# Optimization experiments

Hardware: AMD Instinct MI355X
Metric: run time of the kernel (lower is better)

Reference implementation:

```python
import jax, jax.numpy as jnp
import numpy as np
import math

B, S, DIM = 2, 2048, 2048
NH = 16
HD = DIM // NH  # 128
RANK = 32


def setup_inputs() -> dict:
    key = jax.random.key(0)
    ks = jax.random.split(key, 10)
    x = jax.random.normal(ks[0], (B, S, DIM), dtype=jnp.float32)
    # causal additive mask (use -1e9 instead of -inf for grad-safety)
    mask = jnp.where(jnp.tril(jnp.ones((S, S), dtype=bool)), 0.0, -1e9).astype(jnp.float32)[None, None]
    # rotary frequencies, as in llama: theta = 10000^{-2i/d}
    inv_freq = 1.0 / (10000.0 ** (jnp.arange(0, HD, 2, dtype=jnp.float32) / HD))  # [HD/2]
    t = jnp.arange(S, dtype=jnp.float32)
    freqs = jnp.outer(t, inv_freq)  # [S, HD/2]
    freqs_cos = jnp.cos(freqs)
    freqs_sin = jnp.sin(freqs)
    scale = 0.02
    wq = jax.random.normal(ks[1], (DIM, DIM), dtype=jnp.float32) * scale
    wk = jax.random.normal(ks[2], (DIM, DIM), dtype=jnp.float32) * scale
    wv = jax.random.normal(ks[3], (DIM, DIM), dtype=jnp.float32) * scale
    wo = jax.random.normal(ks[4], (DIM, DIM), dtype=jnp.float32) * scale
    wa_q = jax.random.normal(ks[5], (RANK, DIM), dtype=jnp.float32) * 0.02
    wa_k = jax.random.normal(ks[6], (RANK, DIM), dtype=jnp.float32) * 0.02
    return {"x": x, "mask": mask, "freqs_cos": freqs_cos, "freqs_sin": freqs_sin,
            "wq": wq, "wk": wk, "wv": wv, "wo": wo, "wa_q": wa_q, "wa_k": wa_k}


def _apply_rope(t, cos, sin):
    # t: [B, S, H, HD]; cos/sin: [S, HD/2]
    tr = t.reshape(*t.shape[:-1], HD // 2, 2)
    tre, tim = tr[..., 0], tr[..., 1]
    c = cos[None, :, None, :]
    s = sin[None, :, None, :]
    out_re = tre * c - tim * s
    out_im = tre * s + tim * c
    return jnp.stack([out_re, out_im], axis=-1).reshape(t.shape)


def reference(x, mask, freqs_cos, freqs_sin, wq, wk, wv, wo, wa_q, wa_k):
    bsz, seqlen, dim = x.shape
    xq = (x @ wq.T).reshape(bsz, seqlen, NH, HD)
    xk = (x @ wk.T).reshape(bsz, seqlen, NH, HD)
    xv = (x @ wv.T).reshape(bsz, seqlen, NH, HD)
    # low-rank adaptive gate (computed on detached x in the original)
    xd = jax.lax.stop_gradient(x)
    xq_h = xd @ wa_q.T  # [B, S, 32]
    xk_h = xd @ wa_k.T  # [B, S, 32]
    adaptive_mask = jnp.einsum('bqr,bkr->bqk', xq_h, xk_h)  # [B, S, S]

    xq = _apply_rope(xq, freqs_cos, freqs_sin)
    xk = _apply_rope(xk, freqs_cos, freqs_sin)

    q = xq.transpose(0, 2, 1, 3)  # [B, H, S, HD]
    k = xk.transpose(0, 2, 1, 3)
    v = xv.transpose(0, 2, 1, 3)

    scores = jnp.einsum('bhqd,bhkd->bhqk', q, k) / math.sqrt(HD)
    scores = scores + mask
    scores = jax.nn.softmax(scores.astype(jnp.float32), axis=-1).astype(q.dtype)
    scores = scores * jax.nn.sigmoid(adaptive_mask)[:, None]  # gate, broadcast over heads
    out = jnp.einsum('bhqk,bhkd->bhqd', scores, v)
    out = out.transpose(0, 2, 1, 3).reshape(bsz, seqlen, -1)
    return out @ wo.T
```

## Files before the change

### kernel.cpp

```cpp
#include <hip/hip_runtime.h>

typedef __attribute__((ext_vector_type(8))) short short8v;
typedef __attribute__((ext_vector_type(4))) short short4v;
typedef __attribute__((ext_vector_type(4))) float floatx4;

#define S_    2048
#define DIM_  2048
#define NW_   6400
#define VOFF_ 4352

#define ASG(p) ((__attribute__((address_space(1))) void*)(p))
#define ASL(p) ((__attribute__((address_space(3))) void*)(p))

__device__ __forceinline__ short f2bf(float f){
  union { float f; unsigned u; } c; c.f = f;
  unsigned u = c.u;
  unsigned r = (u + 0x7fffu + ((u >> 16) & 1u)) >> 16;
  return (short)r;
}
__device__ __forceinline__ float bf2f(short s){
  union { unsigned u; float f; } c; c.u = ((unsigned)(unsigned short)s) << 16;
  return c.f;
}

__global__ __launch_bounds__(256) void cvt_k(const float* __restrict__ in,
                                             short* __restrict__ out, int n){
  int i = blockIdx.x*256 + threadIdx.x;
  int idx = i*4;
  if (idx >= n) return;
  floatx4 v = *(const floatx4*)(in + idx);
  short4v o;
  o[0]=f2bf(v[0]); o[1]=f2bf(v[1]); o[2]=f2bf(v[2]); o[3]=f2bf(v[3]);
  *(short4v*)(out + idx) = o;
}

__global__ __launch_bounds__(256)
void cvt_w(const float* wq, const float* waq, const float* wak,
           const float* wk, const float* wv, const float* wo,
           short* Wcat, short* wob){
  const float* src; short* dst; int n;
  switch (blockIdx.y){
    case 0: src=wq;  dst=Wcat;                 n=4194304; break;
    case 1: src=waq; dst=Wcat+(size_t)2048*2048; n=65536; break;
    case 2: src=wak; dst=Wcat+(size_t)2080*2048; n=65536; break;
    case 3: src=wk;  dst=Wcat+(size_t)2112*2048; n=4194304; break;
    case 4: src=wv;  dst=Wcat+(size_t)4352*2048; n=4194304; break;
    case 5: src=wo;  dst=wob;                  n=4194304; break;
    default: {
      int idx = (blockIdx.x*256 + threadIdx.x)*4;
      if (idx < 393216){
        short4v z = {0,0,0,0};
        *(short4v*)(Wcat + (size_t)4160*2048 + idx) = z;
      }
      return;
    }
  }
  int idx = (blockIdx.x*256 + threadIdx.x)*4;
  if (idx >= n) return;
  floatx4 v = *(const floatx4*)(src + idx);
  short4v o;
  o[0]=f2bf(v[0]); o[1]=f2bf(v[1]); o[2]=f2bf(v[2]); o[3]=f2bf(v[3]);
  *(short4v*)(dst + idx) = o;
}

__global__ __launch_bounds__(512,2)
void gemm_qkv(const short* __restrict__ A, const short* __restrict__ B,
              short* __restrict__ Cout, short* __restrict__ Vt){
  __shared__ short SH[65536];
  const int K = 2048;
  int tid = threadIdx.x;
  int wave = tid>>6, lane = tid&63, quad = lane>>4, l16 = lane&15;
  int wm_i = wave>>2, wn_i = wave&3;

  int bid = blockIdx.x;
  int swz = (bid&7)*50 + (bid>>3);
  int m0 = (swz & 15)*256;
  int n0 = (swz >> 4)*256;

  int srow = tid>>2;
  int sseg = (tid&3) ^ ((srow ^ (srow>>2)) & 3);
  const short* aS = A + (size_t)(m0 + srow)*K + sseg*8;
  const short* bS = B + (size_t)(n0 + srow)*K + sseg*8;
  int sdst = wave*512;

  int sx   = (l16 ^ (l16>>2)) & 3;
  int aoff = (wm_i*128 + l16)*32 + (quad^sx)*8;
  int boff = (wn_i*64  + l16)*32 + (quad^sx)*8;

  floatx4 acc[8][4] = {};
  short8v afA[8], afB[8], bfA[4], bfB[4];

#define QSTAGE(src, chunk) do{ \
    __builtin_amdgcn_global_load_lds(ASG(src), ASL(&SH[(chunk)+sdst]), 16, 0, 0); \
    __builtin_amdgcn_global_load_lds(ASG((src) + (size_t)128*2048), ASL(&SH[(chunk)+sdst+4096]), 16, 0, 0); \
  }while(0)
#define QBAR  asm volatile("s_barrier" ::: "memory")
#define QW4   asm volatile("s_waitcnt vmcnt(4)" ::: "memory")
#define MFMA_ __builtin_amdgcn_mfma_f32_16x16x32_bf16

  QSTAGE(aS,            0);
  QSTAGE(bS,        32768);
  QSTAGE(aS+32,      8192);
  QSTAGE(bS+32, 32768+8192);
  QW4;
  QBAR;
  #pragma unroll
  for (int mf=0; mf<4; ++mf) afA[mf] = *(short8v*)&SH[0     + mf*512 + aoff];
  #pragma unroll
  for (int nf=0; nf<4; ++nf) bfA[nf] = *(short8v*)&SH[32768 + nf*512 + boff];
  QSTAGE(aS + 64, 16384);

  for (int t=0; t<32; ++t){
    int buf = t&1, nb = buf^1;
    int A0c = buf*16384,        A1c = A0c+8192;
    int B0c = 32768+buf*16384,  B1c = B0c+8192;
    int A0n = nb*16384,         A1n = A0n+8192;
    int B0n = 32768+nb*16384,   B1n = B0n+8192;
    int kn  = ((t+1)&31)*64;
    int kn2 = ((t+2)&31)*64;

    #pragma unroll
    for (int mf=4; mf<8; ++mf) afA[mf] = *(short8v*)&SH[A0c + mf*512 + aoff];
    QSTAGE(bS + kn, B0n);
    QW4;
    QBAR;
    __builtin_amdgcn_s_setprio(1);
    #pragma unroll
    for (int mf=0; mf<4; ++mf)
      #pragma unroll
      for (int nf=0; nf<4; ++nf)
        acc[mf][nf] = MFMA_(afA[mf], bfA[nf], acc[mf][nf], 0,0,0);
    __builtin_amdgcn_s_setprio(0);

    #pragma unroll
    for (int mf=0; mf<4; ++mf) afB[mf] = *(short8v*)&SH[A1c + mf*512 + aoff];
    #pragma unroll
    for (int nf=0; nf<4; ++nf) bfB[nf] = *(short8v*)&SH[B1c + nf*512 + boff];
    QSTAGE(aS + kn + 32, A1n);
    QBAR;
    __builtin_amdgcn_s_setprio(1);
    #pragma unroll
    for (int mf=4; mf<8; ++mf)
      #pragma unroll
      for (int nf=0; nf<4; ++nf)
        acc[mf][nf] = MFMA_(afA[mf], bfA[nf], acc[mf][nf], 0,0,0);
    __builtin_amdgcn_s_setprio(0);

    #pragma unroll
    for (int mf=4; mf<8; ++mf) afB[mf] = *(short8v*)&SH[A1c + mf*512 + aoff];
    QSTAGE(bS + kn + 32, B1n);
    QW4;
    QBAR;
    __builtin_amdgcn_s_setprio(1);
    #pragma unroll
    for (int mf=0; mf<4; ++mf)
      #pragma unroll
      for (int nf=0; nf<4; ++nf)
        acc[mf][nf] = MFMA_(afB[mf], bfB[nf], acc[mf][nf], 0,0,0);
    __builtin_amdgcn_s_setprio(0);

    #pragma unroll
    for (int mf=0; mf<4; ++mf) afA[mf] = *(short8v*)&SH[A0n + mf*512 + aoff];
    #pragma unroll
    for (int nf=0; nf<4; ++nf) bfA[nf] = *(short8v*)&SH[B0n + nf*512 + boff];
    QSTAGE(aS + kn2, A0c);
    QBAR;
    __builtin_amdgcn_s_setprio(1);
    #pragma unroll
    for (int mf=4; mf<8; ++mf)
      #pragma unroll
      for (int nf=0; nf<4; ++nf)
        acc[mf][nf] = MFMA_(afB[mf], bfB[nf], acc[mf][nf], 0,0,0);
    __builtin_amdgcn_s_setprio(0);
  }

  __syncthreads();

  if (n0 < VOFF_){
    #pragma unroll
    for (int mf=0; mf<8; ++mf)
      #pragma unroll
      for (int r=0; r<4; ++r){
        size_t gm = (size_t)(m0 + wm_i*128 + mf*16 + quad*4 + r);
        #pragma unroll
        for (int nf=0; nf<4; ++nf)
          Cout[gm*NW_ + n0 + wn_i*64 + nf*16 + l16] = f2bf(acc[mf][nf][r]);
      }
  } else {
    short* T = SH;
    #pragma unroll
    for (int mf=0; mf<8; ++mf){
      int mb = wm_i*128 + mf*16 + quad*4;
      int mc = mb>>3, mi = mb&7;
      #pragma unroll
      for (int nf=0; nf<4; ++nf){
        int n = wn_i*64 + nf*16 + l16;
        short4v p;
        p[0]=f2bf(acc[mf][nf][0]); p[1]=f2bf(acc[mf][nf][1]);
        p[2]=f2bf(acc[mf][nf][2]); p[3]=f2bf(acc[mf][nf][3]);
        *(short4v*)&T[n*256 + ((mc ^ (n&31))*8) + mi] = p;
      }
    }
    __syncthreads();
    int f = tid>>1, half = tid&1;
    size_t vbase = (size_t)(n0 - VOFF_ + f)*4096 + m0;
    #pragma unroll
    for (int c=0; c<16; ++c){
      int cc = half*16 + c;
      short8v v = *(short8v*)&T[f*256 + ((cc ^ (f&31))*8)];
      *(short8v*)&Vt[vbase + cc*8] = v;
    }
  }
#undef QSTAGE
#undef QBAR
#undef QW4
#undef MFMA_
}

__global__ __launch_bounds__(256,4)
void gemm_nt_f32(const short* __restrict__ A, const short* __restrict__ B,
                 float* __restrict__ Cout, int M, int N, int K){
  __shared__ short As[128][64];
  __shared__ short Bs[128][64];
  int tid = threadIdx.x;
  int wave = tid>>6, lane = tid&63, quad = lane>>4, l16 = lane&15;
  int l7 = l16&7;
  int m0 = blockIdx.x*128, n0 = blockIdx.y*128;
  int wm = (wave>>1)*64, wn = (wave&1)*64;
  floatx4 acc[4][4] = {};

  int lr = lane>>3;
  int sw = (lane&7) ^ lr;
  const short* Abase = A + (size_t)(m0 + wave*32 + lr)*K + sw*8;
  const short* Bbase = B + (size_t)(n0 + wave*32 + lr)*K + sw*8;

  for (int k0 = 0; k0 < K; k0 += 64){
    __syncthreads();
    #pragma unroll
    for (int i=0;i<4;i++){
      __builtin_amdgcn_global_load_lds(ASG(Abase + (size_t)(i*8)*K + k0),
                                       ASL(&As[wave*32 + i*8][0]), 16, 0, 0);
      __builtin_amdgcn_global_load_lds(ASG(Bbase + (size_t)(i*8)*K + k0),
                                       ASL(&Bs[wave*32 + i*8][0]), 16, 0, 0);
    }
    __syncthreads();
    #pragma unroll
    for (int ks=0; ks<2; ks++){
      short8v af[4], bf[4];
      #pragma unroll
      for (int i=0;i<4;i++) af[i] = *(short8v*)&As[wm + i*16 + l16][((ks*4+quad)^l7)*8];
      #pragma unroll
      for (int j=0;j<4;j++) bf[j] = *(short8v*)&Bs[wn + j*16 + l16][((ks*4+quad)^l7)*8];
      #pragma unroll
      for (int i=0;i<4;i++)
        #pragma unroll
        for (int j=0;j<4;j++)
          acc[i][j] = __builtin_amdgcn_mfma_f32_16x16x32_bf16(af[i], bf[j], acc[i][j], 0,0,0);
    }
  }
  #pragma unroll
  for (int i=0;i<4;i++)
    #pragma unroll
    for (int r=0;r<4;r++){
      int gm = m0 + wm + i*16 + quad*4 + r;
      #pragma unroll
      for (int j=0;j<4;j++){
        int gn = n0 + wn + j*16 + l16;
        Cout[(size_t)gm*N + gn] = acc[i][j][r];
      }
    }
}

__global__ __launch_bounds__(256) void rope_k(short* __restrict__ X,
                                              const float* __restrict__ fcos,
                                              const float* __restrict__ fsin){
  int i = blockIdx.x*256 + threadIdx.x;
  int row = i >> 10;
  int p = i & 1023;
  int s = row & (S_-1);
  int pp = p & 63;
  float c = fcos[s*64+pp], sn = fsin[s*64+pp];
  size_t a = (size_t)row*NW_ + 2112 + p*2;
  int v = *(int*)(X + a);
  float re = bf2f((short)(v & 0xffff)), im = bf2f((short)(v >> 16));
  float orr = re*c - im*sn, oi = re*sn + im*c;
  *(int*)(X + a) = ((int)(unsigned short)f2bf(oi) << 16) | (unsigned short)f2bf(orr);
}

__global__ __launch_bounds__(256)
void gate_k(const short* __restrict__ X, short* __restrict__ G){
  int kt = blockIdx.x, qt = blockIdx.y, b = blockIdx.z;
  if (kt > qt) return;
  int tid = threadIdx.x, wave = tid>>6, lane = tid&63, quad = lane>>4, l16 = lane&15;
  const float NL2E = -1.44269504f;

  short8v qh = *(const short8v*)&X[(size_t)(b*2048 + qt*64 + wave*16 + l16)*NW_ + 2048 + quad*8];
  floatx4 am[4];
  #pragma unroll
  for (int j=0;j<4;j++){
    short8v kh = *(const short8v*)&X[(size_t)(b*2048 + kt*64 + j*16 + l16)*NW_ + 2080 + quad*8];
    floatx4 z = {0.f,0.f,0.f,0.f};
    am[j] = __builtin_amdgcn_mfma_f32_16x16x32_bf16(qh, kh, z, 0,0,0);
  }
  short* Gd = G + (((size_t)(b*32 + kt)*2048) + qt*64 + wave*16 + quad*4)*64 + l16*4;
  #pragma unroll
  for (int r=0;r<4;r++){
    short4v sv;
    #pragma unroll
    for (int j=0;j<4;j++){
      float g = __builtin_amdgcn_rcpf(1.f + __builtin_amdgcn_exp2f(am[j][r]*NL2E));
      sv[j] = f2bf(g);
    }
    *(short4v*)(Gd + (size_t)r*64) = sv;
  }
}

__global__ __launch_bounds__(256,2)
void flash_k(const short* __restrict__ Qc, const short* __restrict__ Vt,
             const short* __restrict__ G, const float* __restrict__ fcos,
             const float* __restrict__ fsin, short* __restrict__ O){
  int h = blockIdx.x, pi = blockIdx.y, b = blockIdx.z;
  int tid = threadIdx.x, wave = tid>>6, lane = tid&63, quad = lane>>4, l16 = lane&15;
  int l7 = l16&7;

  __shared__ short Ks [2][64][128];
  __shared__ short Vts[2][128][64];
  __shared__ short Ps [4][16][72];

  const float CS = 1.44269504f * 0.08838834764831845f;
  int r4 = lane>>4, c16 = lane&15;

#define FSTAGE(kt_, bb) do{ \
    const short* Ksrc = Qc + ((size_t)(b*2048 + (kt_)*64 + wave*16))*NW_ + 2112 + h*128; \
    _Pragma("unroll") \
    for (int j=0;j<4;j++) \
      __builtin_amdgcn_global_load_lds( \
        ASG(Ksrc + (size_t)(j*4 + r4)*NW_ + ((c16 ^ r4 ^ ((j&1)*4))*8)), \
        ASL(&Ks[bb][wave*16 + j*4][0]), 16, 0, 0); \
    const short* Vsrc = Vt + ((size_t)(h*128 + wave*32 + (lane>>3)))*4096 + b*2048 + (kt_)*64 \
                        + (((lane&7) ^ (lane>>3))*8); \
    _Pragma("unroll") \
    for (int j=0;j<4;j++) \
      __builtin_amdgcn_global_load_lds( \
        ASG(Vsrc + (size_t)(j*8)*4096), \
        ASL(&Vts[bb][wave*32 + j*8][0]), 16, 0, 0); \
  }while(0)

  for (int ph = 0; ph < 2; ph++){
    int qt = ph ? pi : 31 - pi;
    int srow = qt*64 + wave*16 + l16;
    size_t qrow = (size_t)(b*2048 + srow);
    short8v qf[4];
    #pragma unroll
    for (int ks=0;ks<4;ks++)
      qf[ks] = *(const short8v*)&Qc[qrow*NW_ + h*128 + ks*32 + quad*8];
    #pragma unroll
    for (int ks=0;ks<4;ks++)
      #pragma unroll
      for (int jj=0;jj<4;jj++){
        float re = bf2f(qf[ks][2*jj]), im = bf2f(qf[ks][2*jj+1]);
        int p = ks*16 + quad*4 + jj;
        float c = fcos[srow*64 + p], sn = fsin[srow*64 + p];
        qf[ks][2*jj]   = f2bf(re*c - im*sn);
        qf[ks][2*jj+1] = f2bf(re*sn + im*c);
      }

    floatx4 oacc[8] = {};
    float lp[4] = {0.f,0.f,0.f,0.f};

    __builtin_amdgcn_s_barrier();
    FSTAGE(0, 0);

    for (int kt=0; kt<=qt; kt++){
      int buf = kt&1;
      asm volatile("s_waitcnt vmcnt(0)" ::: "memory");
      __builtin_amdgcn_s_barrier();

      const short* gb = G + (((size_t)(b*32 + kt)*2048) + qt*64 + wave*16 + quad*4)*64 + l16*4;
      short4v g4[4];
      #pragma unroll
      for (int r=0;r<4;r++) g4[r] = *(const short4v*)(gb + (size_t)r*64);

      if (kt < qt) FSTAGE(kt+1, buf^1);

      floatx4 sacc[4] = {};
      #pragma unroll
      for (int j=0;j<4;j++)
        #pragma unroll
        for (int ks2=0;ks2<4;ks2++){
          short8v kf = *(short8v*)&Ks[buf][j*16+l16][((ks2*4+quad)^l7)*8];
          sacc[j] = __builtin_amdgcn_mfma_f32_16x16x32_bf16(qf[ks2], kf, sacc[j], 0,0,0);
        }

      bool diag = (kt == qt);
      int qbase = wave*16 + quad*4;
      #pragma unroll
      for (int j=0;j<4;j++){
        int kin = j*16 + l16;
        #pragma unroll
        for (int r=0;r<4;r++){
          bool keep = !diag || (kin <= qbase + r);
          float p = keep ? __builtin_amdgcn_exp2f(sacc[j][r]*CS) : 0.f;
          lp[r] += p;
          Ps[wave][quad*4+r][j*16+l16] = f2bf(p * bf2f(g4[r][j]));
        }
      }

      #pragma unroll
      for (int ks2=0; ks2<2; ks2++){
        short8v pf = *(short8v*)&Ps[wave][l16][ks2*32 + quad*8];
        #pragma unroll
        for (int dt=0; dt<8; dt++){
          short8v vf = *(short8v*)&Vts[buf][dt*16 + l16][((ks2*4+quad)^l7)*8];
          oacc[dt] = __builtin_amdgcn_mfma_f32_16x16x32_bf16(pf, vf, oacc[dt], 0,0,0);
        }
      }
    }

    #pragma unroll
    for (int r=0;r<4;r++)
      #pragma unroll
      for (int off=1; off<16; off<<=1)
        lp[r] += __shfl_xor(lp[r], off, 64);
    #pragma unroll
    for (int r=0;r<4;r++){
      float inv = __builtin_amdgcn_rcpf(lp[r]);
      size_t orow = (size_t)(b*2048 + qt*64 + wave*16 + quad*4 + r);
      #pragma unroll
      for (int dt=0;dt<8;dt++)
        O[orow*2048 + h*128 + dt*16 + l16] = f2bf(oacc[dt][r]*inv);
    }
  }
#undef FSTAGE
}

extern "C" void kernel_launch(void* const* d_in, const int* in_sizes, int n_in,
                              void* d_out, int out_size, void* d_ws, size_t ws_size,
                              hipStream_t stream){
  const float* x    = (const float*)d_in[0];
  const float* fcos = (const float*)d_in[2];
  const float* fsin = (const float*)d_in[3];
  const float* wq   = (const float*)d_in[4];
  const float* wk   = (const float*)d_in[5];
  const float* wv   = (const float*)d_in[6];
  const float* wo   = (const float*)d_in[7];
  const float* waq  = (const float*)d_in[8];
  const float* wak  = (const float*)d_in[9];
  float* out = (float*)d_out;

  char* ws = (char*)d_ws;
  size_t off = 0;
  short* xb   = (short*)(ws + off); off += (size_t)4096*2048*2;
  short* Wcat = (short*)(ws + off); off += (size_t)NW_*2048*2;
  short* wob  = (short*)(ws + off); off += (size_t)2048*2048*2;
  short* XQKV = (short*)(ws + off); off += (size_t)4096*NW_*2;
  short* Vtb  = (short*)(ws + off); off += (size_t)2048*4096*2;
  short* G    = xb;
  short* Ob   = Wcat;

  cvt_k<<<8192,256,0,stream>>>(x, xb, 8388608);
  cvt_w<<<dim3(4096,7),256,0,stream>>>(wq, waq, wak, wk, wv, wo, Wcat, wob);

  gemm_qkv<<<dim3(400),512,0,stream>>>(xb, Wcat, XQKV, Vtb);

  rope_k<<<16384,256,0,stream>>>(XQKV, fcos, fsin);
  gate_k<<<dim3(32,32,2),256,0,stream>>>(XQKV, G);

  flash_k<<<dim3(16,16,2),256,0,stream>>>(XQKV, Vtb, G, fcos, fsin, Ob);

  gemm_nt_f32<<<dim3(32,16),256,0,stream>>>(Ob, wob, out, 4096, 2048, 2048);
}
```

Before: 403.6 us.

## Restructure QKV GEMM main loop to split MFMA phases by N fragments

Rewrites the software-pipelined main loop of the fused QKV projection GEMM. It now loads all eight A fragments and half the B fragments per k-substep and computes in two N-halves, instead of the previous cross-iteration A/B double-register prefetch. It adds explicit lgkmcnt(0) waits with scheduling barriers and extra s_barriers around each MFMA phase. This cuts register pressure from the duplicated fragment arrays and simplifies the prefetch schedule, but it adds more barriers and removes some overlap of LDS reads with MFMA.

```diff
diff --git a/kernel.cpp b/kernel.cpp
--- a/kernel.cpp
+++ b/kernel.cpp
@@ -88,7 +88,7 @@
   int boff = (wn_i*64  + l16)*32 + (quad^sx)*8;
 
   floatx4 acc[8][4] = {};
-  short8v afA[8], afB[8], bfA[4], bfB[4];
+  short8v af[8], bf[4];
 
 #define QSTAGE(src, chunk) do{ \
     __builtin_amdgcn_global_load_lds(ASG(src), ASL(&SH[(chunk)+sdst]), 16, 0, 0); \
@@ -96,6 +96,8 @@
   }while(0)
 #define QBAR  asm volatile("s_barrier" ::: "memory")
 #define QW4   asm volatile("s_waitcnt vmcnt(4)" ::: "memory")
+#define QLG   do{ asm volatile("s_waitcnt lgkmcnt(0)" ::: "memory"); \
+                  __builtin_amdgcn_sched_barrier(0); }while(0)
 #define MFMA_ __builtin_amdgcn_mfma_f32_16x16x32_bf16
 
   QSTAGE(aS,            0);
@@ -104,11 +106,6 @@
   QSTAGE(bS+32, 32768+8192);
   QW4;
   QBAR;
-  #pragma unroll
-  for (int mf=0; mf<4; ++mf) afA[mf] = *(short8v*)&SH[0     + mf*512 + aoff];
-  #pragma unroll
-  for (int nf=0; nf<4; ++nf) bfA[nf] = *(short8v*)&SH[32768 + nf*512 + boff];
-  QSTAGE(aS + 64, 16384);
 
   for (int t=0; t<32; ++t){
     int buf = t&1, nb = buf^1;
@@ -117,61 +114,68 @@
     int A0n = nb*16384,         A1n = A0n+8192;
     int B0n = 32768+nb*16384,   B1n = B0n+8192;
     int kn  = ((t+1)&31)*64;
-    int kn2 = ((t+2)&31)*64;
-
-    #pragma unroll
-    for (int mf=4; mf<8; ++mf) afA[mf] = *(short8v*)&SH[A0c + mf*512 + aoff];
+
+    #pragma unroll
+    for (int mf=0; mf<8; ++mf) af[mf] = *(short8v*)&SH[A0c + mf*512 + aoff];
+    bf[0] = *(short8v*)&SH[B0c +   0 + boff];
+    bf[1] = *(short8v*)&SH[B0c + 512 + boff];
+    QSTAGE(aS + kn, A0n);
     QSTAGE(bS + kn, B0n);
+    QBAR;
+    QLG;
+    __builtin_amdgcn_s_setprio(1);
+    #pragma unroll
+    for (int mf=0; mf<8; ++mf){
+      acc[mf][0] = MFMA_(af[mf], bf[0], acc[mf][0], 0,0,0);
+      acc[mf][1] = MFMA_(af[mf], bf[1], acc[mf][1], 0,0,0);
+    }
+    __builtin_amdgcn_s_setprio(0);
+    QBAR;
+
+    bf[2] = *(short8v*)&SH[B0c + 1024 + boff];
+    bf[3] = *(short8v*)&SH[B0c + 1536 + boff];
     QW4;
     QBAR;
+    QLG;
     __builtin_amdgcn_s_setprio(1);
     #pragma unroll
-    for (int mf=0; mf<4; ++mf)
-      #pragma unroll
-      for (int nf=0; nf<4; ++nf)
-        acc[mf][nf] = MFMA_(afA[mf], bfA[nf], acc[mf][nf], 0,0,0);
+    for (int mf=0; mf<8; ++mf){
+      acc[mf][2] = MFMA_(af[mf], bf[2], acc[mf][2], 0,0,0);
+      acc[mf][3] = MFMA_(af[mf], bf[3], acc[mf][3], 0,0,0);
+    }
     __builtin_amdgcn_s_setprio(0);
-
-    #pragma unroll
-    for (int mf=0; mf<4; ++mf) afB[mf] = *(short8v*)&SH[A1c + mf*512 + aoff];
-    #pragma unroll
-    for (int nf=0; nf<4; ++nf) bfB[nf] = *(short8v*)&SH[B1c + nf*512 + boff];
+    QBAR;
+
+    #pragma unroll
+    for (int mf=0; mf<8; ++mf) af[mf] = *(short8v*)&SH[A1c + mf*512 + aoff];
+    bf[0] = *(short8v*)&SH[B1c +   0 + boff];
+    bf[1] = *(short8v*)&SH[B1c + 512 + boff];
     QSTAGE(aS + kn + 32, A1n);
-    QBAR;
+    QSTAGE(bS + kn + 32, B1n);
+    QBAR;
+    QLG;
     __builtin_amdgcn_s_setprio(1);
     #pragma unroll
-    for (int mf=4; mf<8; ++mf)
-      #pragma unroll
-      for (int nf=0; nf<4; ++nf)
-        acc[mf][nf] = MFMA_(afA[mf], bfA[nf], acc[mf][nf], 0,0,0);
+    for (int mf=0; mf<8; ++mf){
+      acc[mf][0] = MFMA_(af[mf], bf[0], acc[mf][0], 0,0,0);
+      acc[mf][1] = MFMA_(af[mf], bf[1], acc[mf][1], 0,0,0);
+    }
     __builtin_amdgcn_s_setprio(0);
-
-    #pragma unroll
-    for (int mf=4; mf<8; ++mf) afB[mf] = *(short8v*)&SH[A1c + mf*512 + aoff];
-    QSTAGE(bS + kn + 32, B1n);
+    QBAR;
+
+    bf[2] = *(short8v*)&SH[B1c + 1024 + boff];
+    bf[3] = *(short8v*)&SH[B1c + 1536 + boff];
     QW4;
     QBAR;
+    QLG;
     __builtin_amdgcn_s_setprio(1);
     #pragma unroll
-    for (int mf=0; mf<4; ++mf)
-      #pragma unroll
-      for (int nf=0; nf<4; ++nf)
-        acc[mf][nf] = MFMA_(afB[mf], bfB[nf], acc[mf][nf], 0,0,0);
+    for (int mf=0; mf<8; ++mf){
+      acc[mf][2] = MFMA_(af[mf], bf[2], acc[mf][2], 0,0,0);
+      acc[mf][3] = MFMA_(af[mf], bf[3], acc[mf][3], 0,0,0);
+    }
     __builtin_amdgcn_s_setprio(0);
-
-    #pragma unroll
-    for (int mf=0; mf<4; ++mf) afA[mf] = *(short8v*)&SH[A0n + mf*512 + aoff];
-    #pragma unroll
-    for (int nf=0; nf<4; ++nf) bfA[nf] = *(short8v*)&SH[B0n + nf*512 + boff];
-    QSTAGE(aS + kn2, A0c);
-    QBAR;
-    __builtin_amdgcn_s_setprio(1);
-    #pragma unroll
-    for (int mf=4; mf<8; ++mf)
-      #pragma unroll
-      for (int nf=0; nf<4; ++nf)
-        acc[mf][nf] = MFMA_(afB[mf], bfB[nf], acc[mf][nf], 0,0,0);
-    __builtin_amdgcn_s_setprio(0);
+    QBAR;
   }
 
   __syncthreads();
@@ -214,6 +218,7 @@
 #undef QSTAGE
 #undef QBAR
 #undef QW4
+#undef QLG
 #undef MFMA_
 }
 
```

New measurement: 433.3 us. +7.3%, slower.
